# Performance work log

Hardware: AMD Instinct MI355X
Metric: run time of the kernel (lower is better)

Reference implementation:

```python
import jax, jax.numpy as jnp
import numpy as np

# Module config (from init_kwargs)
H_IN, W_IN = 512, 512      # input_shape
H_OUT, W_OUT = 512, 512    # output_shape
SMOOTHING = 2
LOG_POLAR_DISTANCE = 2.0   # 'circumscribed' position
BATCH, CHANNELS = 32, 3


def setup_inputs() -> dict:
    key = jax.random.key(0)
    data = jax.random.normal(key, (BATCH, CHANNELS, H_IN, W_IN), dtype=jnp.float32)
    return {"data": data}


def _compute_map():
    # MAX_R = log(||input_shape|| / 2 * log_polar_distance)  (circumscribed)
    max_r = np.float32(np.log(np.linalg.norm([float(H_IN), float(W_IN)]) / 2.0 * LOG_POLAR_DISTANCE))
    theta, r = jnp.meshgrid(jnp.arange(H_OUT, dtype=jnp.float32),
                            jnp.arange(W_OUT, dtype=jnp.float32), indexing='ij')
    radius = jnp.exp(r * max_r / W_OUT)                 # [H_OUT, W_OUT]
    X = radius * jnp.cos(theta * 2.0 * jnp.pi / H_OUT)
    Y = radius * jnp.sin(theta * 2.0 * jnp.pi / H_OUT)
    return X, Y


def reference(data):
    X0, Y0 = _compute_map()
    center_y, center_x = H_IN / 2.0, W_IN / 2.0  # default_center
    X = center_x + X0
    Y = center_y - Y0
    # compute_mask uses input_shape[0] bound for X and input_shape[1] for Y (as in source)
    mask = ((0 <= X) & (X < H_IN) & (0 <= Y) & (Y < W_IN)).astype(data.dtype)

    # .long() in torch truncates toward zero; astype(int32) matches, then clamp.
    y_down = jnp.clip(Y.astype(jnp.int32), 0, H_IN - 1)
    x_down = jnp.clip(X.astype(jnp.int32), 0, W_IN - 1)
    y_up = jnp.clip(y_down + 1, 0, H_IN - 1)
    x_up = jnp.clip(x_down + 1, 0, W_IN - 1)

    yd = Y - y_down.astype(Y.dtype)
    yu = Y - y_up.astype(Y.dtype)
    xd = X - x_down.astype(X.dtype)
    xu = X - x_up.astype(X.dtype)
    dd = yd ** SMOOTHING + xd ** SMOOTHING
    du = yd ** SMOOTHING + xu ** SMOOTHING
    ud = yu ** SMOOTHING + xd ** SMOOTHING
    uu = yu ** SMOOTHING + xu ** SMOOTHING
    total = dd + du + ud + uu

    # Four gathers over the trailing (H,W) dims -> [B, C, H_OUT, W_OUT]
    out = mask * ((dd / total) * data[..., y_down, x_down]
                  + (du / total) * data[..., y_down, x_up]
                  + (ud / total) * data[..., y_up, x_down]
                  + (uu / total) * data[..., y_up, x_up])
    return out
```

## Files before the change

kernel.cpp:

```cpp
#include <hip/hip_runtime.h>
#include <math.h>


constexpr int H_IN  = 512;
constexpr int W_IN  = 512;
constexpr int H_OUT = 512;
constexpr int W_OUT = 512;
constexpr int BC    = 32 * 3;
constexpr int IMG   = H_IN * W_IN;
constexpr int NCHUNK = 8;
constexpr int IPC   = BC / NCHUNK;

__device__ __forceinline__ float2 ld2(const float* p) {
    float2 v;
    __builtin_memcpy(&v, p, sizeof(v));
    return v;
}

__global__ __launch_bounds__(256) void logpolar_kernel(
    const float* __restrict__ data, float* __restrict__ out)
{
    const int chunk = blockIdx.x & (NCHUNK - 1);
    const int tile  = blockIdx.x >> 3;
    const int tile_i = (tile >> 5) << 4;
    const int tile_j = (tile & 31) << 4;

    const int t = threadIdx.x;
    const int w = t >> 6;
    const int l = t & 63;
    const int i = tile_i + ((w >> 1) << 3) + (l >> 3);
    const int j = tile_j + ((w & 1) << 3) + (l & 7);
    const int pix = (i << 9) | j;

    const float max_r = (float)6.584898215319481;

    const float theta  = ((float)(2 * i) * 3.14159274101257324f) / (float)H_OUT;
    const float radius = expf(((float)j * max_r) / (float)W_OUT);
    const float X = 256.0f + radius * cosf(theta);
    const float Y = 256.0f - radius * sinf(theta);

    const float* p = data + (size_t)chunk * IPC * IMG;
    float*       q = out  + (size_t)chunk * IPC * IMG + pix;

    const bool in_bounds =
        (X >= 0.0f) && (X < (float)H_IN) && (Y >= 0.0f) && (Y < (float)W_IN);

    if (!in_bounds) {
        #pragma unroll
        for (int bc = 0; bc < IPC; ++bc) q[bc * IMG] = 0.0f;
        return;
    }

    const int y_down = (int)Y;
    const int x_down = (int)X;
    const int y_up = min(y_down + 1, H_IN - 1);
    const int x_up = min(x_down + 1, W_IN - 1);

    const float yd = Y - (float)y_down;
    const float yu = Y - (float)y_up;
    const float xd = X - (float)x_down;
    const float xu = X - (float)x_up;

    const float dd = yd * yd + xd * xd;
    const float du = yd * yd + xu * xu;
    const float ud = yu * yu + xd * xd;
    const float uu = yu * yu + xu * xu;
    const float total = ((dd + du) + ud) + uu;

    const float wdd = dd / total;
    const float wdu = du / total;
    const float wud = ud / total;
    const float wuu = uu / total;

    const int o_d = y_down * W_IN + x_down;
    const int o_u = y_up   * W_IN + x_down;

    if (x_down < W_IN - 1) {
        #pragma unroll 4
        for (int bc = 0; bc < IPC; ++bc) {
            const float* pp = p + bc * IMG;
            const float2 a = ld2(pp + o_d);
            const float2 b = ld2(pp + o_u);
            q[bc * IMG] = ((wdd * a.x + wdu * a.y) + wud * b.x) + wuu * b.y;
        }
    } else {
        #pragma unroll 4
        for (int bc = 0; bc < IPC; ++bc) {
            const float* pp = p + bc * IMG;
            const float ga = pp[o_d];
            const float gb = pp[o_u];
            q[bc * IMG] = ((wdd * ga + wdu * ga) + wud * gb) + wuu * gb;
        }
    }
}

extern "C" void kernel_launch(void* const* d_in, const int* in_sizes, int n_in,
                              void* d_out, int out_size, void* d_ws, size_t ws_size,
                              hipStream_t stream)
{
    const float* data = (const float*)d_in[0];
    float* out = (float*)d_out;

    const int threads = 256;
    const int blocks = (H_OUT / 16) * (W_OUT / 16) * NCHUNK;
    logpolar_kernel<<<blocks, threads, 0, stream>>>(data, out);
}
```

Measured before the change: 242.5 us.

## Stage per-tile input bounding box in LDS before bilinear gather

Each block now computes the bounding box of source pixels its 16x16 output tile needs, using wave shuffles plus an LDS reduction. For each image it loads that box into shared memory with coalesced row reads and serves the four-tap gathers from LDS. Tiles with too wide a footprint fall back to the direct global gather. The thread mapping also changes to a row-major 16x16 layout. The aim is to replace scattered, uncoalesced global loads with coalesced ones. The cost is two barriers per image, loop-carried prefetching and extra LDS traffic, and for small-radius tiles the box loads may fetch more data than the gather needs.

Measured after the change: 289.1 us. +19.2%, slower.

```diff
diff --git a/kernel.cpp b/kernel.cpp
--- a/kernel.cpp
+++ b/kernel.cpp
@@ -1,15 +1,15 @@
 #include <hip/hip_runtime.h>
 #include <math.h>
+#include <limits.h>
 
 
 constexpr int H_IN  = 512;
 constexpr int W_IN  = 512;
-constexpr int H_OUT = 512;
-constexpr int W_OUT = 512;
 constexpr int BC    = 32 * 3;
 constexpr int IMG   = H_IN * W_IN;
 constexpr int NCHUNK = 8;
 constexpr int IPC   = BC / NCHUNK;
+constexpr int LDS_FLOATS = 8192;
 
 __device__ __forceinline__ float2 ld2(const float* p) {
     float2 v;
@@ -20,6 +20,9 @@
 __global__ __launch_bounds__(256) void logpolar_kernel(
     const float* __restrict__ data, float* __restrict__ out)
 {
+    __shared__ float smem[LDS_FLOATS];
+    __shared__ int red[16];
+
     const int chunk = blockIdx.x & (NCHUNK - 1);
     const int tile  = blockIdx.x >> 3;
     const int tile_i = (tile >> 5) << 4;
@@ -28,31 +31,23 @@
     const int t = threadIdx.x;
     const int w = t >> 6;
     const int l = t & 63;
-    const int i = tile_i + ((w >> 1) << 3) + (l >> 3);
-    const int j = tile_j + ((w & 1) << 3) + (l & 7);
+    const int row = t >> 4;
+    const int col = t & 15;
+    const int i = tile_i + row;
+    const int j = tile_j + col;
     const int pix = (i << 9) | j;
 
     const float max_r = (float)6.584898215319481;
-
-    const float theta  = ((float)(2 * i) * 3.14159274101257324f) / (float)H_OUT;
-    const float radius = expf(((float)j * max_r) / (float)W_OUT);
+    const float theta  = ((float)(2 * i) * 3.14159274101257324f) / 512.0f;
+    const float radius = expf(((float)j * max_r) / 512.0f);
     const float X = 256.0f + radius * cosf(theta);
     const float Y = 256.0f - radius * sinf(theta);
 
-    const float* p = data + (size_t)chunk * IPC * IMG;
-    float*       q = out  + (size_t)chunk * IPC * IMG + pix;
+    const bool ib =
+        (X >= 0.0f) && (X < 512.0f) && (Y >= 0.0f) && (Y < 512.0f);
 
-    const bool in_bounds =
-        (X >= 0.0f) && (X < (float)H_IN) && (Y >= 0.0f) && (Y < (float)W_IN);
-
-    if (!in_bounds) {
-        #pragma unroll
-        for (int bc = 0; bc < IPC; ++bc) q[bc * IMG] = 0.0f;
-        return;
-    }
-
-    const int y_down = (int)Y;
-    const int x_down = (int)X;
+    const int y_down = ib ? (int)Y : 0;
+    const int x_down = ib ? (int)X : 0;
     const int y_up = min(y_down + 1, H_IN - 1);
     const int x_up = min(x_down + 1, W_IN - 1);
 
@@ -60,36 +55,118 @@
     const float yu = Y - (float)y_up;
     const float xd = X - (float)x_down;
     const float xu = X - (float)x_up;
-
     const float dd = yd * yd + xd * xd;
     const float du = yd * yd + xu * xu;
     const float ud = yu * yu + xd * xd;
     const float uu = yu * yu + xu * xu;
     const float total = ((dd + du) + ud) + uu;
-
     const float wdd = dd / total;
     const float wdu = du / total;
     const float wud = ud / total;
     const float wuu = uu / total;
 
-    const int o_d = y_down * W_IN + x_down;
-    const int o_u = y_up   * W_IN + x_down;
+    int ymn = ib ? y_down : INT_MAX;
+    int ymx = ib ? y_up   : INT_MIN;
+    int xmn = ib ? x_down : INT_MAX;
+    int xmx = ib ? x_up   : INT_MIN;
+    #pragma unroll
+    for (int m = 1; m < 64; m <<= 1) {
+        ymn = min(ymn, __shfl_xor(ymn, m));
+        ymx = max(ymx, __shfl_xor(ymx, m));
+        xmn = min(xmn, __shfl_xor(xmn, m));
+        xmx = max(xmx, __shfl_xor(xmx, m));
+    }
+    if (l == 0) {
+        red[w * 4 + 0] = ymn; red[w * 4 + 1] = ymx;
+        red[w * 4 + 2] = xmn; red[w * 4 + 3] = xmx;
+    }
+    __syncthreads();
+    ymn = min(min(red[0], red[4]), min(red[8],  red[12]));
+    ymx = max(max(red[1], red[5]), max(red[9],  red[13]));
+    xmn = min(min(red[2], red[6]), min(red[10], red[14]));
+    xmx = max(max(red[3], red[7]), max(red[11], red[15]));
 
-    if (x_down < W_IN - 1) {
-        #pragma unroll 4
+    const float* p = data + (size_t)chunk * IPC * IMG;
+    float*       q = out  + (size_t)chunk * IPC * IMG + pix;
+
+    if (ymx == INT_MIN) {
+        #pragma unroll
+        for (int bc = 0; bc < IPC; ++bc) q[bc * IMG] = 0.0f;
+        return;
+    }
+
+    const int Hb = ymx - ymn + 1;
+    const int Wb = xmx - xmn + 1;
+    const bool narrow = (Wb <= 64);
+    const int S = narrow ? 65 : 129;
+
+    if (Wb <= 128 && (Hb + 1) * S <= LDS_FLOATS) {
+        const int o  = ib ? ((y_down - ymn) * S + (x_down - xmn)) : 0;
+        const bool cx = (x_up > x_down);
+        const bool cy = (y_up > y_down);
+        const int cg0 = xmn + min(l, Wb - 1);
+        const int cg1 = xmn + min(l + 64, Wb - 1);
+
         for (int bc = 0; bc < IPC; ++bc) {
-            const float* pp = p + bc * IMG;
-            const float2 a = ld2(pp + o_d);
-            const float2 b = ld2(pp + o_u);
-            q[bc * IMG] = ((wdd * a.x + wdu * a.y) + wud * b.x) + wuu * b.y;
+            const float* img = p + bc * IMG;
+            if (narrow) {
+                int r = w;
+                float v0 = img[(ymn + min(r, Hb - 1)) * 512 + cg0];
+                while (r < Hb) {
+                    const int rn = r + 4;
+                    const float v1 = img[(ymn + min(rn, Hb - 1)) * 512 + cg0];
+                    smem[r * 65 + l] = v0;
+                    v0 = v1; r = rn;
+                }
+            } else {
+                int r = w;
+                int rg = (ymn + min(r, Hb - 1)) * 512;
+                float v0 = img[rg + cg0];
+                float u0 = img[rg + cg1];
+                while (r < Hb) {
+                    const int rn = r + 4;
+                    rg = (ymn + min(rn, Hb - 1)) * 512;
+                    const float v1 = img[rg + cg0];
+                    const float u1 = img[rg + cg1];
+                    smem[r * 129 + l] = v0;
+                    smem[r * 129 + 64 + l] = u0;
+                    v0 = v1; u0 = u1; r = rn;
+                }
+            }
+            __syncthreads();
+            const float a0 = smem[o];
+            const float a1 = smem[o + 1];
+            const float b0 = smem[o + S];
+            const float b1 = smem[o + S + 1];
+            const float fdu = cx ? a1 : a0;
+            const float fud = cy ? b0 : a0;
+            const float fuu = cy ? (cx ? b1 : b0) : fdu;
+            const float v = ((wdd * a0 + wdu * fdu) + wud * fud) + wuu * fuu;
+            q[bc * IMG] = ib ? v : 0.0f;
+            __syncthreads();
         }
     } else {
-        #pragma unroll 4
-        for (int bc = 0; bc < IPC; ++bc) {
-            const float* pp = p + bc * IMG;
-            const float ga = pp[o_d];
-            const float gb = pp[o_u];
-            q[bc * IMG] = ((wdd * ga + wdu * ga) + wud * gb) + wuu * gb;
+        const int o_d = y_down * 512 + x_down;
+        const int o_u = y_up   * 512 + x_down;
+        if (!ib) {
+            #pragma unroll
+            for (int bc = 0; bc < IPC; ++bc) q[bc * IMG] = 0.0f;
+        } else if (x_up > x_down) {
+            #pragma unroll 4
+            for (int bc = 0; bc < IPC; ++bc) {
+                const float* pp = p + bc * IMG;
+                const float2 a = ld2(pp + o_d);
+                const float2 b = ld2(pp + o_u);
+                q[bc * IMG] = ((wdd * a.x + wdu * a.y) + wud * b.x) + wuu * b.y;
+            }
+        } else {
+            #pragma unroll
+            for (int bc = 0; bc < IPC; ++bc) {
+                const float* pp = p + bc * IMG;
+                const float ga = pp[o_d];
+                const float gb = pp[o_u];
+                q[bc * IMG] = ((wdd * ga + wdu * ga) + wud * gb) + wuu * gb;
+            }
         }
     }
 }
@@ -102,6 +179,6 @@
     float* out = (float*)d_out;
 
     const int threads = 256;
-    const int blocks = (H_OUT / 16) * (W_OUT / 16) * NCHUNK;
+    const int blocks = (512 / 16) * (512 / 16) * NCHUNK;
     logpolar_kernel<<<blocks, threads, 0, stream>>>(data, out);
 }
```
